# Kernel optimization log

Hardware: AMD Instinct MI355X
Metric: run time of the kernel (lower is better)

## Reference

```python
import jax, jax.numpy as jnp
import numpy as np

T, B = 32, 8192
M, N = 4, 2          # state dim, obs dim (hardcoded in source)
H1, HID, H2 = 480, 200, 320


def _l2norm(x):
    # tf.nn.l2_normalize(x, axis=1, epsilon=1e-12)
    return x / jnp.sqrt(jnp.maximum(jnp.sum(x * x, axis=1, keepdims=True), 1e-12))


def _gru_step(x, h, Wg, Ug, bg):
    # keras GRU cell, reset_after=True (default): separate input/recurrent biases
    xm = x @ Wg + bg[0]
    hm = h @ Ug + bg[1]
    xz, xr, xh = jnp.split(xm, 3, axis=1)
    hz, hr, hh = jnp.split(hm, 3, axis=1)
    z = jax.nn.sigmoid(xz + hz)
    r = jax.nn.sigmoid(xr + hr)
    hcand = jnp.tanh(xh + r * hh)
    return z * h + (1.0 - z) * hcand


def setup_inputs() -> dict:
    key = jax.random.key(0)
    ks = jax.random.split(key, 10)
    y = jax.random.normal(ks[0], (T, B, N), jnp.float32)
    # Stable dynamics so the filter does not blow up over T steps
    F = 0.9 * jnp.eye(M, dtype=jnp.float32) + 0.05 * jax.random.normal(ks[1], (M, M), jnp.float32)
    Hm = 0.5 * jax.random.normal(ks[2], (N, M), jnp.float32)
    W1 = jax.random.normal(ks[3], (M + 2 * N, H1), jnp.float32) / jnp.sqrt(8.0)
    b1 = jnp.zeros((H1,), jnp.float32)
    Wg = jax.random.normal(ks[4], (H1, 3 * HID), jnp.float32) / jnp.sqrt(float(H1))
    Ug = jax.random.normal(ks[5], (HID, 3 * HID), jnp.float32) / jnp.sqrt(float(HID))
    bg = jnp.zeros((2, 3 * HID), jnp.float32)
    W2 = jax.random.normal(ks[6], (HID, H2), jnp.float32) / jnp.sqrt(float(HID))
    b2 = jnp.zeros((H2,), jnp.float32)
    W3 = 0.02 * jax.random.normal(ks[7], (H2, M * N), jnp.float32) / jnp.sqrt(float(H2))
    b3 = jnp.zeros((M * N,), jnp.float32)
    hn0 = jax.random.normal(ks[8], (B, HID), jnp.float32)
    return dict(y=y, F=F, Hm=Hm, W1=W1, b1=b1, Wg=Wg, Ug=Ug, bg=bg,
                W2=W2, b2=b2, W3=W3, b3=b3, hn0=hn0)


def reference(y, F, Hm, W1, b1, Wg, Ug, bg, W2, b2, W3, b3, hn0):
    def step(carry, yt):
        m1x_prior, m1x_post, hn = carry                      # [B,M],[B,M],[B,HID]
        m1x_prev_prior = m1x_prior
        m1x_prior = jnp.einsum('ij,bj->bi', F, m1x_post)     # F @ posterior
        m1y = jnp.einsum('ij,bj->bi', Hm, m1x_prior)         # H @ prior
        dm1x_norm = _l2norm(m1x_post - m1x_prev_prior)       # [B,M]
        dm1y = yt - m1y                                      # [B,N]
        dm1y_norm = _l2norm(dm1y)
        # NOTE: source normalizes dm1y (not dm1y_f1) for the second feature -- kept faithful
        knet_in = jnp.concatenate([dm1y_norm, dm1y_norm, dm1x_norm], axis=1)  # [B,8]
        a1 = jax.nn.relu(knet_in @ W1 + b1)                  # [B,H1]
        hn = _gru_step(a1, hn, Wg, Ug, bg)                   # [B,HID]
        a2 = jax.nn.relu(hn @ W2 + b2)                       # [B,H2]
        KG = (a2 @ W3 + b3).reshape(-1, M, N)                # [B,M,N]
        inov = jnp.einsum('bmn,bn->bm', KG, dm1y)            # KGain @ dy
        m1x_post = m1x_prior + inov
        return (m1x_prior, m1x_post, hn), m1x_post

    init = (jnp.zeros((B, M), y.dtype), jnp.zeros((B, M), y.dtype), hn0)
    _, xs = jax.lax.scan(step, init, y)
    return xs  # [T,B,M] posterior state estimates (squeezed)
```

## Files before the change

kernel.cpp:

```cpp
#include <hip/hip_runtime.h>


namespace {

constexpr int T_STEPS = 32;
constexpr int BATCH   = 8192;
constexpr int H1      = 480;
constexpr int HID     = 200;
constexpr int H2      = 320;
constexpr int BR      = 32;
constexpr int NTHR    = 1024;
constexpr int KTG     = 22;
constexpr int KTA     = 15;
constexpr int NTG     = 52;
constexpr int NTW1    = 30;
constexpr int NT2     = 20;
constexpr int KT2     = 7;
constexpr int KT3     = 10;

using f16x8 = __attribute__((ext_vector_type(8))) _Float16;
using f32x4 = __attribute__((ext_vector_type(4))) float;

__device__ _Float16 g_w1[NTW1 * 512];
__device__ _Float16 g_wcat[NTG * KTG * 512];
__device__ _Float16 g_w2[NT2 * KT2 * 512];
__device__ _Float16 g_w3[KT3 * 512];

#define MFMA16(A, B, C) __builtin_amdgcn_mfma_f32_16x16x32_f16((A), (B), (C), 0, 0, 0)
#define SBAR() __builtin_amdgcn_sched_barrier(0)

__device__ __forceinline__ float sigmoid_(float x) { return 1.f / (1.f + __expf(-x)); }
__device__ __forceinline__ float tanh_(float x) {
  x = fminf(fmaxf(x, -15.f), 15.f);
  const float e = __expf(-2.f * x);
  return (1.f - e) / (1.f + e);
}
__device__ __forceinline__ f16x8 f16x8_zero() {
  f16x8 v;
#pragma unroll
  for (int i = 0; i < 8; ++i) v[i] = (_Float16)0.f;
  return v;
}

__device__ __forceinline__ int fragoff(int k, int r) {
  const int kt = k >> 5, kk = k & 31;
  return kt * 1024 + ((r >> 4) * 512) + ((((kk >> 3) << 4) | (r & 15)) * 8) + (kk & 7);
}

__global__ __launch_bounds__(256) void prep_kernel(
    const float* __restrict__ W1, const float* __restrict__ b1,
    const float* __restrict__ Wg, const float* __restrict__ Ug,
    const float* __restrict__ W2, const float* __restrict__ b2,
    const float* __restrict__ W3) {
  const int idx = blockIdx.x * 256 + threadIdx.x;
  constexpr int TOTW1 = NTW1 * 512;
  constexpr int TOT1  = NTG * KTG * 512;
  constexpr int TOT2  = NT2 * KT2 * 512;
  constexpr int TOT3  = KT3 * 512;
  if (idx < TOTW1) {
    const int i = idx & 7, l = (idx >> 3) & 63, nt = idx >> 9;
    const int g = l >> 4, c = l & 15;
    const int k = g * 8 + i, col = nt * 16 + c;
    float wv = 0.f;
    if (k < 8) wv = W1[k * H1 + col];
    else if (k == 8) wv = b1[col];
    g_w1[idx] = (_Float16)wv;
  } else if (idx < TOTW1 + TOT1) {
    const int id = idx - TOTW1;
    const int i = id & 7, l = (id >> 3) & 63, nk = id >> 9;
    const int kt = nk % KTG, nt = nk / KTG;
    const int g = l >> 4, c = l & 15;
    const int k = kt * 32 + g * 8 + i;
    const int grp = nt / 13;
    const int jj = (nt - grp * 13) * 16 + c;
    float wv = 0.f;
    if (jj < HID) {
      if (grp == 0) {
        if (k < H1) wv = Wg[k * 600 + jj];
        else if (k < H1 + HID) wv = Ug[(k - H1) * 600 + jj];
      } else if (grp == 1) {
        if (k < H1) wv = Wg[k * 600 + 200 + jj];
        else if (k < H1 + HID) wv = Ug[(k - H1) * 600 + 200 + jj];
      } else if (grp == 2) {
        if (k < H1) wv = Wg[k * 600 + 400 + jj];
      } else {
        if (k >= H1 && k < H1 + HID) wv = Ug[(k - H1) * 600 + 400 + jj];
      }
    }
    g_wcat[id] = (_Float16)wv;
  } else if (idx < TOTW1 + TOT1 + TOT2) {
    const int id = idx - TOTW1 - TOT1;
    const int i = id & 7, l = (id >> 3) & 63, nk = id >> 9;
    const int kt = nk % KT2, nt = nk / KT2;
    const int g = l >> 4, c = l & 15;
    const int k = kt * 32 + g * 8 + i;
    const int col = nt * 16 + c;
    float wv = 0.f;
    if (k < HID) wv = W2[k * H2 + col];
    else if (k == 200) wv = b2[col];
    g_w2[id] = (_Float16)wv;
  } else if (idx < TOTW1 + TOT1 + TOT2 + TOT3) {
    const int id = idx - TOTW1 - TOT1 - TOT2;
    const int i = id & 7, l = (id >> 3) & 63, kt = id >> 9;
    const int g = l >> 4, c = l & 15;
    const int k = kt * 32 + g * 8 + i;
    g_w3[id] = (_Float16)((c < 8) ? W3[k * 8 + c] : 0.f);
  }
}

__global__
__attribute__((amdgpu_flat_work_group_size(NTHR, NTHR)))
__attribute__((amdgpu_waves_per_eu(4, 4)))
void knet_kernel(
    const float* __restrict__ y,
    const float* __restrict__ Fm,
    const float* __restrict__ Hm,
    const float* __restrict__ bg,
    const float* __restrict__ b3,
    const float* __restrict__ hn0,
    float* __restrict__ out)
{
  __shared__ alignas(16) _Float16 sA1[KTA * 2 * 512];
  __shared__ alignas(16) _Float16 sAhh[KT2 * 2 * 512];
  __shared__ alignas(16) _Float16 sAhl[KT2 * 2 * 512];
  __shared__ alignas(16) float s_in8T[8][BR];
  __shared__ alignas(16) float s_kgp[2][BR][8];
  __shared__ alignas(16) float s_bias[4][HID];
  __shared__ alignas(16) float s_fh[32];
  __shared__ alignas(16) float s_b3[8];
  __shared__ alignas(16) float s_prior2[2][BR][4];
  __shared__ alignas(16) float s_d2[2][BR][2];

  const int tid  = threadIdx.x;
  const int lane = tid & 63;
  const int wid  = __builtin_amdgcn_readfirstlane(tid >> 6);
  const int row0 = blockIdx.x * BR;
  const int rl   = lane & 31;
  const int g4   = (lane >> 4) << 2;
  const int ab   = lane * 8;
  const int c16  = lane & 15;

  if (tid < HID) {
    s_bias[0][tid] = bg[tid]       + bg[600 + tid];
    s_bias[1][tid] = bg[200 + tid] + bg[800 + tid];
    s_bias[2][tid] = bg[400 + tid];
    s_bias[3][tid] = bg[1000 + tid];
  }
  if (tid < 16) s_fh[tid] = Fm[tid];
  else if (tid < 24) s_fh[tid] = Hm[tid - 16];
  if (tid < 8) s_b3[tid] = b3[tid];
  if (tid < BR * 4) s_prior2[0][tid >> 2][tid & 3] = 0.f;
  if (tid < BR * 2) s_d2[0][tid >> 1][tid & 1] = 0.f;
  for (int e = tid; e < HID * BR; e += NTHR) {
    const int j = e >> 5, r = e & 31;
    const float h0 = hn0[(size_t)(row0 + r) * HID + j];
    const int off = fragoff(j, r);
    const _Float16 hi = (_Float16)h0;
    sAhh[off] = hi;
    sAhl[off] = (_Float16)(h0 - (float)hi);
  }
  for (int e = tid; e < 24 * BR; e += NTHR) {
    const int kh = 200 + (e >> 5), r = e & 31;
    const int off = fragoff(kh, r);
    sAhh[off] = (_Float16)((kh == 200) ? 1.f : 0.f);
    sAhl[off] = (_Float16)0.f;
  }
  __syncthreads();

  for (int t = 0; t < T_STEPS; ++t) {
    const int p = t & 1;
    {
      float post[4] = {0.f, 0.f, 0.f, 0.f};
      if (t > 0) {
        float kg[8];
#pragma unroll
        for (int cc = 0; cc < 8; ++cc)
          kg[cc] = s_kgp[0][rl][cc] + s_kgp[1][rl][cc] + s_b3[cc];
        const float pd0 = s_d2[p][rl][0], pd1 = s_d2[p][rl][1];
#pragma unroll
        for (int m = 0; m < 4; ++m)
          post[m] = s_prior2[p][rl][m] + kg[2 * m] * pd0 + kg[2 * m + 1] * pd1;
        if (wid == 0 && lane < BR) {
          float4 o; o.x = post[0]; o.y = post[1]; o.z = post[2]; o.w = post[3];
          *(float4*)&out[((size_t)(t - 1) * BATCH + row0 + rl) * 4] = o;
        }
      }
      float opri[4], np[4];
#pragma unroll
      for (int m = 0; m < 4; ++m) opri[m] = s_prior2[p][rl][m];
#pragma unroll
      for (int m = 0; m < 4; ++m) {
        float s = 0.f;
#pragma unroll
        for (int j = 0; j < 4; ++j) s += s_fh[m * 4 + j] * post[j];
        np[m] = s;
      }
      float m0 = 0.f, m1 = 0.f;
#pragma unroll
      for (int m = 0; m < 4; ++m) { m0 += s_fh[16 + m] * np[m]; m1 += s_fh[20 + m] * np[m]; }
      const float2 yv = *(const float2*)&y[((size_t)t * BATCH + row0 + rl) * 2];
      const float d0 = yv.x - m0;
      const float d1 = yv.y - m1;
      float dx[4], ssx = 0.f;
#pragma unroll
      for (int m = 0; m < 4; ++m) { dx[m] = post[m] - opri[m]; ssx += dx[m] * dx[m]; }
      const float idx_ = rsqrtf(fmaxf(ssx, 1e-12f));
      const float idy_ = rsqrtf(fmaxf(d0 * d0 + d1 * d1, 1e-12f));
      if (lane < BR) {
#pragma unroll
        for (int m = 0; m < 4; ++m) s_prior2[p ^ 1][rl][m] = np[m];
        s_d2[p ^ 1][rl][0] = d0;
        s_d2[p ^ 1][rl][1] = d1;
        const float n0 = d0 * idy_, n1 = d1 * idy_;
        s_in8T[0][rl] = n0; s_in8T[1][rl] = n1;
        s_in8T[2][rl] = n0; s_in8T[3][rl] = n1;
#pragma unroll
        for (int m = 0; m < 4; ++m) s_in8T[4 + m][rl] = dx[m] * idx_;
      }
    }
    {
      f16x8 ah0 = f16x8_zero(), al0 = f16x8_zero();
      f16x8 ah1 = f16x8_zero(), al1 = f16x8_zero();
      const int g = lane >> 4;
      if (g == 0) {
#pragma unroll
        for (int i = 0; i < 8; ++i) {
          const float v0 = s_in8T[i][c16];
          const float v1 = s_in8T[i][c16 + 16];
          const _Float16 h0 = (_Float16)v0; ah0[i] = h0; al0[i] = (_Float16)(v0 - (float)h0);
          const _Float16 h1 = (_Float16)v1; ah1[i] = h1; al1[i] = (_Float16)(v1 - (float)h1);
        }
      } else if (g == 1) {
        ah0[0] = (_Float16)1.f;
        ah1[0] = (_Float16)1.f;
      }
      f32x4 p00 = {0.f, 0.f, 0.f, 0.f}, p01 = p00, p10 = p00, p11 = p00;
      const f16x8 w1a = *(const f16x8*)&g_w1[(size_t)wid * 512 + ab];
      p00 = MFMA16(ah0, w1a, p00); p00 = MFMA16(al0, w1a, p00);
      p01 = MFMA16(ah1, w1a, p01); p01 = MFMA16(al1, w1a, p01);
      const bool hasB = (wid < 14);
      if (hasB) {
        const f16x8 w1b = *(const f16x8*)&g_w1[(size_t)(16 + wid) * 512 + ab];
        p10 = MFMA16(ah0, w1b, p10); p10 = MFMA16(al0, w1b, p10);
        p11 = MFMA16(ah1, w1b, p11); p11 = MFMA16(al1, w1b, p11);
      }
#define ASTORE1(A0, A1, COLBASE)                                     \
      { const int col = (COLBASE) + c16;                             \
        _Pragma("unroll")                                            \
        for (int reg = 0; reg < 4; ++reg) {                          \
          sA1[fragoff(col, g4 + reg)]      = (_Float16)fmaxf(A0[reg], 0.f); \
          sA1[fragoff(col, 16 + g4 + reg)] = (_Float16)fmaxf(A1[reg], 0.f); \
        } }
      ASTORE1(p00, p01, wid * 16)
      if (hasB) ASTORE1(p10, p11, (16 + wid) * 16)
    }
    __syncthreads();

    f32x4 aZ0 = {0.f, 0.f, 0.f, 0.f}, aZ1 = aZ0, aR0 = aZ0, aR1 = aZ0;
    f32x4 aX0 = aZ0, aX1 = aZ0, aH0 = aZ0, aH1 = aZ0;
    if (wid < 13) {
      const _Float16* bzp = g_wcat + ((size_t)(0  + wid) * KTG) * 512 + ab;
      const _Float16* brp = g_wcat + ((size_t)(13 + wid) * KTG) * 512 + ab;
      const _Float16* bxp = g_wcat + ((size_t)(26 + wid) * KTG) * 512 + ab;
      const _Float16* bhp = g_wcat + ((size_t)(39 + wid) * KTG) * 512 + ab;
#define LD3(KT) (((KT) < KTA) ? *(const f16x8*)(bxp + (KT) * 512) \
                              : *(const f16x8*)(bhp + (KT) * 512))
      f16x8 bzC = *(const f16x8*)(bzp);
      f16x8 brC = *(const f16x8*)(brp);
      f16x8 bxC = LD3(0);
#pragma unroll
      for (int kt = 0; kt < KTG; ++kt) {
        f16x8 bzN, brN, bxN;
        if (kt + 1 < KTG) {
          bzN = *(const f16x8*)(bzp + (kt + 1) * 512);
          brN = *(const f16x8*)(brp + (kt + 1) * 512);
          bxN = LD3(kt + 1);
        }
        if (kt < KTA) {
          const int _o = kt * 1024 + ab;
          const f16x8 ca0 = *(const f16x8*)&sA1[_o];
          const f16x8 ca1 = *(const f16x8*)&sA1[_o + 512];
          SBAR();
          aZ0 = MFMA16(ca0, bzC, aZ0);
          aZ1 = MFMA16(ca1, bzC, aZ1);
          aR0 = MFMA16(ca0, brC, aR0);
          aR1 = MFMA16(ca1, brC, aR1);
          aX0 = MFMA16(ca0, bxC, aX0);
          aX1 = MFMA16(ca1, bxC, aX1);
        } else {
          const int _o = (kt - KTA) * 1024 + ab;
          const f16x8 cah0 = *(const f16x8*)&sAhh[_o];
          const f16x8 cal0 = *(const f16x8*)&sAhl[_o];
          const f16x8 cah1 = *(const f16x8*)&sAhh[_o + 512];
          const f16x8 cal1 = *(const f16x8*)&sAhl[_o + 512];
          SBAR();
          aZ0 = MFMA16(cah0, bzC, aZ0);  aZ0 = MFMA16(cal0, bzC, aZ0);
          aZ1 = MFMA16(cah1, bzC, aZ1);  aZ1 = MFMA16(cal1, bzC, aZ1);
          aR0 = MFMA16(cah0, brC, aR0);  aR0 = MFMA16(cal0, brC, aR0);
          aR1 = MFMA16(cah1, brC, aR1);  aR1 = MFMA16(cal1, brC, aR1);
          aH0 = MFMA16(cah0, bxC, aH0);  aH0 = MFMA16(cal0, bxC, aH0);
          aH1 = MFMA16(cah1, bxC, aH1);  aH1 = MFMA16(cal1, bxC, aH1);
        }
        if (kt + 1 < KTG) { bzC = bzN; brC = brN; bxC = bxN; }
      }
#undef LD3
    }
    __syncthreads();

    if (wid < 13) {
      const int j = wid * 16 + c16;
      if (j < HID) {
        const float bz  = s_bias[0][j], brb = s_bias[1][j];
        const float bxh = s_bias[2][j], bhh = s_bias[3][j];
#define GRU1(AZ, AR, AX, AH, MB)                                         \
        _Pragma("unroll")                                                \
        for (int reg = 0; reg < 4; ++reg) {                              \
          const int r = (MB) * 16 + g4 + reg;                            \
          const int off = fragoff(j, r);                                 \
          const float hold = (float)sAhh[off] + (float)sAhl[off];        \
          const float z  = sigmoid_(AZ[reg] + bz);                       \
          const float rr = sigmoid_(AR[reg] + brb);                      \
          const float hc = tanh_((AX[reg] + bxh) + rr * (AH[reg] + bhh));\
          const float hn = z * hold + (1.f - z) * hc;                    \
          const _Float16 qh = (_Float16)hn;                              \
          sAhh[off] = qh;                                                \
          sAhl[off] = (_Float16)(hn - (float)qh);                       \
        }
        GRU1(aZ0, aR0, aX0, aH0, 0)
        GRU1(aZ1, aR1, aX1, aH1, 1)
#undef GRU1
      }
    }
    __syncthreads();

    {
      f32x4 e00 = {0.f, 0.f, 0.f, 0.f}, e01 = e00, e10 = e00, e11 = e00;
      const _Float16* w2a = g_w2 + ((size_t)wid * KT2) * 512 + ab;
      const _Float16* w2b = g_w2 + ((size_t)(16 + wid) * KT2) * 512 + ab;
      f16x8 baC = *(const f16x8*)(w2a);
      f16x8 bbC = (wid < 4) ? *(const f16x8*)(w2b) : f16x8_zero();
#pragma unroll
      for (int qt = 0; qt < KT2; ++qt) {
        const int _o = qt * 1024 + ab;
        const f16x8 cah0 = *(const f16x8*)&sAhh[_o];
        const f16x8 cal0 = *(const f16x8*)&sAhl[_o];
        const f16x8 cah1 = *(const f16x8*)&sAhh[_o + 512];
        const f16x8 cal1 = *(const f16x8*)&sAhl[_o + 512];
        f16x8 baN, bbN;
        if (qt + 1 < KT2) {
          baN = *(const f16x8*)(w2a + (qt + 1) * 512);
          if (wid < 4) bbN = *(const f16x8*)(w2b + (qt + 1) * 512);
        }
        SBAR();
        e00 = MFMA16(cah0, baC, e00); e00 = MFMA16(cal0, baC, e00);
        e01 = MFMA16(cah1, baC, e01); e01 = MFMA16(cal1, baC, e01);
        if (wid < 4) {
          e10 = MFMA16(cah0, bbC, e10); e10 = MFMA16(cal0, bbC, e10);
          e11 = MFMA16(cah1, bbC, e11); e11 = MFMA16(cal1, bbC, e11);
        }
        if (qt + 1 < KT2) { baC = baN; if (wid < 4) bbC = bbN; }
      }
      ASTORE1(e00, e01, wid * 16)
      if (wid < 4) ASTORE1(e10, e11, (16 + wid) * 16)
#undef ASTORE1
    }
    __syncthreads();

    if (wid < 4) {
      const int mB = wid & 1, half = wid >> 1;
      f32x4 ka = {0.f, 0.f, 0.f, 0.f};
      const _Float16* w3p = g_w3 + ab;
#pragma unroll
      for (int q = 0; q < 5; ++q) {
        const int kt3 = half * 5 + q;
        const int _o = kt3 * 1024 + mB * 512 + ab;
        const f16x8 a  = *(const f16x8*)&sA1[_o];
        const f16x8 bw = *(const f16x8*)(w3p + kt3 * 512);
        ka = MFMA16(a, bw, ka);
      }
      if (c16 < 8) {
        const int rb = mB * 16 + g4;
#pragma unroll
        for (int reg = 0; reg < 4; ++reg) s_kgp[half][rb + reg][c16] = ka[reg];
      }
    }
    __syncthreads();
  }

  {
    float kg[8];
#pragma unroll
    for (int cc = 0; cc < 8; ++cc)
      kg[cc] = s_kgp[0][rl][cc] + s_kgp[1][rl][cc] + s_b3[cc];
    const float pd0 = s_d2[0][rl][0], pd1 = s_d2[0][rl][1];
    if (wid == 0 && lane < BR) {
      float4 o;
      o.x = s_prior2[0][rl][0] + kg[0] * pd0 + kg[1] * pd1;
      o.y = s_prior2[0][rl][1] + kg[2] * pd0 + kg[3] * pd1;
      o.z = s_prior2[0][rl][2] + kg[4] * pd0 + kg[5] * pd1;
      o.w = s_prior2[0][rl][3] + kg[6] * pd0 + kg[7] * pd1;
      *(float4*)&out[((size_t)(T_STEPS - 1) * BATCH + row0 + rl) * 4] = o;
    }
  }
}

}

extern "C" void kernel_launch(void* const* d_in, const int* in_sizes, int n_in,
                              void* d_out, int out_size, void* d_ws, size_t ws_size,
                              hipStream_t stream) {
  const float* y   = (const float*)d_in[0];
  const float* Fm  = (const float*)d_in[1];
  const float* Hm  = (const float*)d_in[2];
  const float* W1  = (const float*)d_in[3];
  const float* b1  = (const float*)d_in[4];
  const float* Wg  = (const float*)d_in[5];
  const float* Ug  = (const float*)d_in[6];
  const float* bg  = (const float*)d_in[7];
  const float* W2  = (const float*)d_in[8];
  const float* b2  = (const float*)d_in[9];
  const float* W3  = (const float*)d_in[10];
  const float* b3  = (const float*)d_in[11];
  const float* hn0 = (const float*)d_in[12];
  float* out = (float*)d_out;

  constexpr int PREP_TOT = (NTW1 + NTG * KTG + NT2 * KT2 + KT3) * 512;
  prep_kernel<<<(PREP_TOT + 255) / 256, 256, 0, stream>>>(W1, b1, Wg, Ug, W2, b2, W3);
  knet_kernel<<<BATCH / BR, NTHR, 0, stream>>>(y, Fm, Hm, bg, b3, hn0, out);
}
```

Measured before the change: 1.210 ms.

## Overlap layer-1 MFMA on idle warps with recurrent GRU matmul on others

Warp specialization: the 3 warps that are idle during the gate GEMM (wid>=13) now compute the whole first layer (input features times W1, ReLU, store to sA1). At the same time, warps 0-12 run the recurrent-state part of the gate GEMM (hidden state times Ug), which does not depend on sA1. Once both finish, warps 0-12 do the input part over sA1. The aim is to hide layer-1 latency behind the recurrent matmul. The cost is an extra barrier and serialising layer 1 over 10 tiles on only 3 warps.

```diff
diff --git a/kernel.cpp b/kernel.cpp
--- a/kernel.cpp
+++ b/kernel.cpp
@@ -218,32 +218,8 @@
         for (int m = 0; m < 4; ++m) s_in8T[4 + m][rl] = dx[m] * idx_;
       }
     }
-    {
-      f16x8 ah0 = f16x8_zero(), al0 = f16x8_zero();
-      f16x8 ah1 = f16x8_zero(), al1 = f16x8_zero();
-      const int g = lane >> 4;
-      if (g == 0) {
-#pragma unroll
-        for (int i = 0; i < 8; ++i) {
-          const float v0 = s_in8T[i][c16];
-          const float v1 = s_in8T[i][c16 + 16];
-          const _Float16 h0 = (_Float16)v0; ah0[i] = h0; al0[i] = (_Float16)(v0 - (float)h0);
-          const _Float16 h1 = (_Float16)v1; ah1[i] = h1; al1[i] = (_Float16)(v1 - (float)h1);
-        }
-      } else if (g == 1) {
-        ah0[0] = (_Float16)1.f;
-        ah1[0] = (_Float16)1.f;
-      }
-      f32x4 p00 = {0.f, 0.f, 0.f, 0.f}, p01 = p00, p10 = p00, p11 = p00;
-      const f16x8 w1a = *(const f16x8*)&g_w1[(size_t)wid * 512 + ab];
-      p00 = MFMA16(ah0, w1a, p00); p00 = MFMA16(al0, w1a, p00);
-      p01 = MFMA16(ah1, w1a, p01); p01 = MFMA16(al1, w1a, p01);
-      const bool hasB = (wid < 14);
-      if (hasB) {
-        const f16x8 w1b = *(const f16x8*)&g_w1[(size_t)(16 + wid) * 512 + ab];
-        p10 = MFMA16(ah0, w1b, p10); p10 = MFMA16(al0, w1b, p10);
-        p11 = MFMA16(ah1, w1b, p11); p11 = MFMA16(al1, w1b, p11);
-      }
+    __syncthreads();
+
 #define ASTORE1(A0, A1, COLBASE)                                     \
       { const int col = (COLBASE) + c16;                             \
         _Pragma("unroll")                                            \
@@ -251,59 +227,96 @@
           sA1[fragoff(col, g4 + reg)]      = (_Float16)fmaxf(A0[reg], 0.f); \
           sA1[fragoff(col, 16 + g4 + reg)] = (_Float16)fmaxf(A1[reg], 0.f); \
         } }
-      ASTORE1(p00, p01, wid * 16)
-      if (hasB) ASTORE1(p10, p11, (16 + wid) * 16)
-    }
-    __syncthreads();
 
     f32x4 aZ0 = {0.f, 0.f, 0.f, 0.f}, aZ1 = aZ0, aR0 = aZ0, aR1 = aZ0;
     f32x4 aX0 = aZ0, aX1 = aZ0, aH0 = aZ0, aH1 = aZ0;
+    const _Float16* bzp = g_wcat + ((size_t)(0  + wid) * KTG) * 512 + ab;
+    const _Float16* brp = g_wcat + ((size_t)(13 + wid) * KTG) * 512 + ab;
+    const _Float16* bxp = g_wcat + ((size_t)(26 + wid) * KTG) * 512 + ab;
+    const _Float16* bhp = g_wcat + ((size_t)(39 + wid) * KTG) * 512 + ab;
+
+    if (wid >= 13) {
+      f16x8 ah0 = f16x8_zero(), al0 = f16x8_zero();
+      f16x8 ah1 = f16x8_zero(), al1 = f16x8_zero();
+      const int g = lane >> 4;
+      if (g == 0) {
+#pragma unroll
+        for (int i = 0; i < 8; ++i) {
+          const float v0 = s_in8T[i][c16];
+          const float v1 = s_in8T[i][c16 + 16];
+          const _Float16 h0 = (_Float16)v0; ah0[i] = h0; al0[i] = (_Float16)(v0 - (float)h0);
+          const _Float16 h1 = (_Float16)v1; ah1[i] = h1; al1[i] = (_Float16)(v1 - (float)h1);
+        }
+      } else if (g == 1) {
+        ah0[0] = (_Float16)1.f;
+        ah1[0] = (_Float16)1.f;
+      }
+      const int t0 = wid - 13;
+      f16x8 wC = *(const f16x8*)&g_w1[(size_t)t0 * 512 + ab];
+#pragma unroll
+      for (int u = 0; u < 10; ++u) {
+        f16x8 wN;
+        if (u + 1 < 10) wN = *(const f16x8*)&g_w1[(size_t)(t0 + 3 * (u + 1)) * 512 + ab];
+        SBAR();
+        f32x4 q0 = {0.f, 0.f, 0.f, 0.f}, q1 = q0;
+        q0 = MFMA16(ah0, wC, q0); q0 = MFMA16(al0, wC, q0);
+        q1 = MFMA16(ah1, wC, q1); q1 = MFMA16(al1, wC, q1);
+        ASTORE1(q0, q1, (t0 + 3 * u) * 16)
+        if (u + 1 < 10) wC = wN;
+      }
+    } else {
+      f16x8 bzC = *(const f16x8*)(bzp + 15 * 512);
+      f16x8 brC = *(const f16x8*)(brp + 15 * 512);
+      f16x8 bhC = *(const f16x8*)(bhp + 15 * 512);
+#pragma unroll
+      for (int kh = 0; kh < 7; ++kh) {
+        f16x8 bzN, brN, bhN;
+        if (kh + 1 < 7) {
+          bzN = *(const f16x8*)(bzp + (16 + kh) * 512);
+          brN = *(const f16x8*)(brp + (16 + kh) * 512);
+          bhN = *(const f16x8*)(bhp + (16 + kh) * 512);
+        }
+        const int _o = kh * 1024 + ab;
+        const f16x8 cah0 = *(const f16x8*)&sAhh[_o];
+        const f16x8 cal0 = *(const f16x8*)&sAhl[_o];
+        const f16x8 cah1 = *(const f16x8*)&sAhh[_o + 512];
+        const f16x8 cal1 = *(const f16x8*)&sAhl[_o + 512];
+        SBAR();
+        aZ0 = MFMA16(cah0, bzC, aZ0);  aZ0 = MFMA16(cal0, bzC, aZ0);
+        aZ1 = MFMA16(cah1, bzC, aZ1);  aZ1 = MFMA16(cal1, bzC, aZ1);
+        aR0 = MFMA16(cah0, brC, aR0);  aR0 = MFMA16(cal0, brC, aR0);
+        aR1 = MFMA16(cah1, brC, aR1);  aR1 = MFMA16(cal1, brC, aR1);
+        aH0 = MFMA16(cah0, bhC, aH0);  aH0 = MFMA16(cal0, bhC, aH0);
+        aH1 = MFMA16(cah1, bhC, aH1);  aH1 = MFMA16(cal1, bhC, aH1);
+        if (kh + 1 < 7) { bzC = bzN; brC = brN; bhC = bhN; }
+      }
+    }
+    __syncthreads();
+
     if (wid < 13) {
-      const _Float16* bzp = g_wcat + ((size_t)(0  + wid) * KTG) * 512 + ab;
-      const _Float16* brp = g_wcat + ((size_t)(13 + wid) * KTG) * 512 + ab;
-      const _Float16* bxp = g_wcat + ((size_t)(26 + wid) * KTG) * 512 + ab;
-      const _Float16* bhp = g_wcat + ((size_t)(39 + wid) * KTG) * 512 + ab;
-#define LD3(KT) (((KT) < KTA) ? *(const f16x8*)(bxp + (KT) * 512) \
-                              : *(const f16x8*)(bhp + (KT) * 512))
       f16x8 bzC = *(const f16x8*)(bzp);
       f16x8 brC = *(const f16x8*)(brp);
-      f16x8 bxC = LD3(0);
-#pragma unroll
-      for (int kt = 0; kt < KTG; ++kt) {
+      f16x8 bxC = *(const f16x8*)(bxp);
+#pragma unroll
+      for (int kt = 0; kt < KTA; ++kt) {
         f16x8 bzN, brN, bxN;
-        if (kt + 1 < KTG) {
+        if (kt + 1 < KTA) {
           bzN = *(const f16x8*)(bzp + (kt + 1) * 512);
           brN = *(const f16x8*)(brp + (kt + 1) * 512);
-          bxN = LD3(kt + 1);
-        }
-        if (kt < KTA) {
-          const int _o = kt * 1024 + ab;
-          const f16x8 ca0 = *(const f16x8*)&sA1[_o];
-          const f16x8 ca1 = *(const f16x8*)&sA1[_o + 512];
-          SBAR();
-          aZ0 = MFMA16(ca0, bzC, aZ0);
-          aZ1 = MFMA16(ca1, bzC, aZ1);
-          aR0 = MFMA16(ca0, brC, aR0);
-          aR1 = MFMA16(ca1, brC, aR1);
-          aX0 = MFMA16(ca0, bxC, aX0);
-          aX1 = MFMA16(ca1, bxC, aX1);
-        } else {
-          const int _o = (kt - KTA) * 1024 + ab;
-          const f16x8 cah0 = *(const f16x8*)&sAhh[_o];
-          const f16x8 cal0 = *(const f16x8*)&sAhl[_o];
-          const f16x8 cah1 = *(const f16x8*)&sAhh[_o + 512];
-          const f16x8 cal1 = *(const f16x8*)&sAhl[_o + 512];
-          SBAR();
-          aZ0 = MFMA16(cah0, bzC, aZ0);  aZ0 = MFMA16(cal0, bzC, aZ0);
-          aZ1 = MFMA16(cah1, bzC, aZ1);  aZ1 = MFMA16(cal1, bzC, aZ1);
-          aR0 = MFMA16(cah0, brC, aR0);  aR0 = MFMA16(cal0, brC, aR0);
-          aR1 = MFMA16(cah1, brC, aR1);  aR1 = MFMA16(cal1, brC, aR1);
-          aH0 = MFMA16(cah0, bxC, aH0);  aH0 = MFMA16(cal0, bxC, aH0);
-          aH1 = MFMA16(cah1, bxC, aH1);  aH1 = MFMA16(cal1, bxC, aH1);
-        }
-        if (kt + 1 < KTG) { bzC = bzN; brC = brN; bxC = bxN; }
-      }
-#undef LD3
+          bxN = *(const f16x8*)(bxp + (kt + 1) * 512);
+        }
+        const int _o = kt * 1024 + ab;
+        const f16x8 ca0 = *(const f16x8*)&sA1[_o];
+        const f16x8 ca1 = *(const f16x8*)&sA1[_o + 512];
+        SBAR();
+        aZ0 = MFMA16(ca0, bzC, aZ0);
+        aZ1 = MFMA16(ca1, bzC, aZ1);
+        aR0 = MFMA16(ca0, brC, aR0);
+        aR1 = MFMA16(ca1, brC, aR1);
+        aX0 = MFMA16(ca0, bxC, aX0);
+        aX1 = MFMA16(ca1, bxC, aX1);
+        if (kt + 1 < KTA) { bzC = bzN; brC = brN; bxC = bxN; }
+      }
     }
     __syncthreads();
 
```

Measured after the change: 1.729 ms. 1.43x slower.
